# Kernel tuning notes

Measured on AMD Instinct MI355X. Metric: run time of the kernel, lower is better.

The kernel has to match this reference:

```python
import jax, jax.numpy as jnp
import numpy as np

N_NODES = 50000


def gcn_conv(x, W, b, edge_index, n):
    """PyG GCNConv with add_self_loops=True, normalize=True (symmetric norm)."""
    loop = jnp.arange(n, dtype=edge_index.dtype)
    row = jnp.concatenate([edge_index[0], loop])  # source
    col = jnp.concatenate([edge_index[1], loop])  # target
    ones = jnp.ones(row.shape[0], dtype=x.dtype)
    deg = jax.ops.segment_sum(ones, col, num_segments=n)
    dinv = jnp.where(deg > 0, jax.lax.rsqrt(deg), 0.0)
    norm = dinv[row] * dinv[col]  # [E+N]
    h = x @ W  # [N, hidden]
    out = jax.ops.segment_sum(h[row] * norm[:, None], col, num_segments=n)
    return out + b


def hgcn_forward(x, ei_ppi, ei_go, W0_ppi, b0_ppi, W0_go, b0_go,
                 W1_ppi, b1_ppi, W1_go, b1_go, Wc, bc, cand_edge_index):
    n = x.shape[0]
    # layer 0: HeteroConv(aggr='mean') over the two relations, then ReLU
    h = 0.5 * (gcn_conv(x, W0_ppi, b0_ppi, ei_ppi, n)
               + gcn_conv(x, W0_go, b0_go, ei_go, n))
    h = jax.nn.relu(h)
    # layer 1
    h = 0.5 * (gcn_conv(h, W1_ppi, b1_ppi, ei_ppi, n)
               + gcn_conv(h, W1_go, b1_go, ei_go, n))
    z = jax.nn.relu(h)  # [N, hidden]
    src, dst = cand_edge_index
    h_pair = jnp.concatenate([z[src], z[dst]], axis=1)  # [P, 2*hidden]
    logits = h_pair @ Wc + bc
    return z, jax.nn.sigmoid(logits)


def setup_inputs() -> dict:
    key = jax.random.key(0)
    ks = jax.random.split(key, 12)
    n, in_dim, hid, out_dim, E, P = N_NODES, 256, 128, 2, 1_000_000, 131072
    s = 1.0 / np.sqrt(in_dim)
    s2 = 1.0 / np.sqrt(hid)
    sc = 1.0 / np.sqrt(2 * hid)
    return {
        "x": jax.random.normal(ks[0], (n, in_dim), jnp.float32),
        "ei_ppi": jax.random.randint(ks[1], (2, E), 0, n, jnp.int32),
        "ei_go": jax.random.randint(ks[2], (2, E), 0, n, jnp.int32),
        "cand_edge_index": jax.random.randint(ks[3], (2, P), 0, n, jnp.int32),
        "W0_ppi": jax.random.normal(ks[4], (in_dim, hid), jnp.float32) * s,
        "b0_ppi": jnp.zeros((hid,), jnp.float32),
        "W0_go": jax.random.normal(ks[5], (in_dim, hid), jnp.float32) * s,
        "b0_go": jnp.zeros((hid,), jnp.float32),
        "W1_ppi": jax.random.normal(ks[6], (hid, hid), jnp.float32) * s2,
        "b1_ppi": jnp.zeros((hid,), jnp.float32),
        "W1_go": jax.random.normal(ks[7], (hid, hid), jnp.float32) * s2,
        "b1_go": jnp.zeros((hid,), jnp.float32),
        "Wc": jax.random.normal(ks[8], (2 * hid, out_dim), jnp.float32) * sc,
        "bc": jnp.zeros((out_dim,), jnp.float32),
    }


def reference(x, ei_ppi, ei_go, cand_edge_index, W0_ppi, b0_ppi, W0_go, b0_go,
              W1_ppi, b1_ppi, W1_go, b1_go, Wc, bc):
    return hgcn_forward(x, ei_ppi, ei_go, W0_ppi, b0_ppi, W0_go, b0_go,
                        W1_ppi, b1_ppi, W1_go, b1_go, Wc, bc, cand_edge_index)
```

## Files before the change

### kernel.cpp

```cpp
#include <hip/hip_runtime.h>
#include <math.h>

typedef _Float16 f16;
typedef f16  f16x2 __attribute__((ext_vector_type(2)));
typedef f16  f16x8 __attribute__((ext_vector_type(8)));
typedef float f32x4 __attribute__((ext_vector_type(4)));

#define CAP 64
#define CHK 96

__global__ __launch_bounds__(256) void prep3_kernel(
        int* __restrict__ cnt_p, const int* __restrict__ cols_p, const int* __restrict__ rows_p, int E1,
        int* __restrict__ cnt_g, const int* __restrict__ cols_g, const int* __restrict__ rows_g, int E2,
        unsigned short* __restrict__ buf_p, unsigned short* __restrict__ buf_g,
        const float* __restrict__ x, f16* __restrict__ xh, int x8,
        const float* __restrict__ W0p, const float* __restrict__ W0g,
        const float* __restrict__ W1p, const float* __restrict__ W1g,
        f16* __restrict__ T0p, f16* __restrict__ T0g,
        f16* __restrict__ T1p, f16* __restrict__ T1g,
        f16* __restrict__ zrow_p, f16* __restrict__ zrow_g,
        int XB, int n) {
    const int b = blockIdx.x;
    const int EBLK = 2 * CHK * 8;
    if (b < EBLK) {
        const int owner   = b & 7;
        const int pairIdx = b >> 3;
        const int sel     = (pairIdx >= CHK);
        const int chunk   = pairIdx - (sel ? CHK : 0);
        const int* cols = sel ? cols_g : cols_p;
        const int* rows = sel ? rows_g : rows_p;
        int* cnt = sel ? cnt_g : cnt_p;
        unsigned short* buf = sel ? buf_g : buf_p;
        const int E = sel ? E2 : E1;
        const int csz  = (((E + CHK - 1) / CHK) + 3) & ~3;
        const int s    = chunk * csz;
        const int eend = (s + csz < E) ? (s + csz) : E;
        if (s >= E) return;
        const int rlo = (int)((size_t)owner * n / 8);
        const int rhi = (int)((size_t)(owner + 1) * n / 8);
        const int vecEnd = s + ((eend - s) & ~3);
        for (int e = s + threadIdx.x * 4; e < vecEnd; e += 1024) {
            int4 c4 = *(const int4*)(cols + e);
            int4 r4 = *(const int4*)(rows + e);
            if (c4.x >= rlo && c4.x < rhi) {
                int p = atomicAdd(&cnt[c4.x], 1);
                if (p < CAP) buf[(size_t)c4.x * CAP + p] = (unsigned short)r4.x;
            }
            if (c4.y >= rlo && c4.y < rhi) {
                int p = atomicAdd(&cnt[c4.y], 1);
                if (p < CAP) buf[(size_t)c4.y * CAP + p] = (unsigned short)r4.y;
            }
            if (c4.z >= rlo && c4.z < rhi) {
                int p = atomicAdd(&cnt[c4.z], 1);
                if (p < CAP) buf[(size_t)c4.z * CAP + p] = (unsigned short)r4.z;
            }
            if (c4.w >= rlo && c4.w < rhi) {
                int p = atomicAdd(&cnt[c4.w], 1);
                if (p < CAP) buf[(size_t)c4.w * CAP + p] = (unsigned short)r4.w;
            }
        }
        for (int e = vecEnd + threadIdx.x; e < eend; e += 256) {
            int c = cols[e];
            if (c >= rlo && c < rhi) {
                int p = atomicAdd(&cnt[c], 1);
                if (p < CAP) buf[(size_t)c * CAP + p] = (unsigned short)rows[e];
            }
        }
    } else if (b < EBLK + XB) {
        int i = (b - EBLK) * 256 + threadIdx.x;
        if (i < x8) {
            const float4* p = (const float4*)(x + (size_t)i * 8);
            float4 a = p[0], c = p[1];
            f16x8 v = { (f16)a.x, (f16)a.y, (f16)a.z, (f16)a.w,
                        (f16)c.x, (f16)c.y, (f16)c.z, (f16)c.w };
            *(f16x8*)(xh + (size_t)i * 8) = v;
        }
    } else {
        int idx = (b - EBLK - XB) * 256 + threadIdx.x;
        if (idx < 98304) {
            const float* W; f16* T; int K; int local;
            if (idx < 32768)      { W = W0p; T = T0p; K = 256; local = idx; }
            else if (idx < 65536) { W = W0g; T = T0g; K = 256; local = idx - 32768; }
            else if (idx < 81920) { W = W1p; T = T1p; K = 128; local = idx - 65536; }
            else                  { W = W1g; T = T1g; K = 128; local = idx - 81920; }
            int k = local >> 7, nn = local & 127;
            T[(size_t)nn * K + k] = (f16)W[local];
        } else if (idx < 98304 + 256) {
            int t = idx - 98304;
            f16x8 zv = {};
            if (t < 16)       *(f16x8*)(zrow_p + t * 8) = zv;
            else if (t < 32)  *(f16x8*)(zrow_g + (t - 16) * 8) = zv;
        }
    }
}

__global__ __launch_bounds__(256) void gemm_dual_kernel(const f16* __restrict__ A,
        const f16* __restrict__ Btp, const f16* __restrict__ Btg,
        const int* __restrict__ cnt_p, const int* __restrict__ cnt_g,
        f16* __restrict__ Cp, f16* __restrict__ Cg, int M, int K) {
    const int wave = threadIdx.x >> 6;
    const int lane = threadIdx.x & 63;
    const int m    = lane & 15;
    const int kq   = lane >> 4;
    const int row0 = blockIdx.x * 64 + wave * 16;

    int arow = row0 + m; if (arow >= M) arow = M - 1;
    const f16* ap = A + (size_t)arow * K + kq * 8;

    f32x4 accp[8], accg[8];
    #pragma unroll
    for (int t = 0; t < 8; t++) {
        accp[t] = (f32x4){0.0f, 0.0f, 0.0f, 0.0f};
        accg[t] = (f32x4){0.0f, 0.0f, 0.0f, 0.0f};
    }
    for (int k0 = 0; k0 < K; k0 += 32) {
        f16x8 a = *(const f16x8*)(ap + k0);
        #pragma unroll
        for (int t = 0; t < 8; t++) {
            f16x8 bp = *(const f16x8*)(Btp + (size_t)(t * 16 + m) * K + k0 + kq * 8);
            accp[t] = __builtin_amdgcn_mfma_f32_16x16x32_f16(a, bp, accp[t], 0, 0, 0);
            f16x8 bg = *(const f16x8*)(Btg + (size_t)(t * 16 + m) * K + k0 + kq * 8);
            accg[t] = __builtin_amdgcn_mfma_f32_16x16x32_f16(a, bg, accg[t], 0, 0, 0);
        }
    }
    #pragma unroll
    for (int r = 0; r < 4; r++) {
        int row = row0 + kq * 4 + r;
        if (row < M) {
            float sp = rsqrtf(1.0f + (float)cnt_p[row]);
            float sg = rsqrtf(1.0f + (float)cnt_g[row]);
            #pragma unroll
            for (int t = 0; t < 8; t++) {
                Cp[(size_t)row * 128 + t * 16 + m] = (f16)(accp[t][r] * sp);
                Cg[(size_t)row * 128 + t * 16 + m] = (f16)(accg[t][r] * sg);
            }
        }
    }
}

template<int OUTF32>
__global__ __launch_bounds__(256) void fused_agg_kernel(
        const f16* __restrict__ Ap, const f16* __restrict__ Ag,
        const int* __restrict__ cnt_p, const unsigned short* __restrict__ buf_p,
        const int* __restrict__ cnt_g, const unsigned short* __restrict__ buf_g,
        const float* __restrict__ b_p, const float* __restrict__ b_g,
        float* __restrict__ outf, f16* __restrict__ outh, f16* __restrict__ outh2, int n) {
    const int wave = (blockIdx.x * blockDim.x + threadIdx.x) >> 6;
    const int lane = threadIdx.x & 63;
    if (wave >= n) return;
    const int c  = wave;
    const int g  = lane >> 4;
    const int sl = lane & 15;
    const size_t fo = (size_t)sl * 8;

    float ap[8] = {}, ag[8] = {};

    {
        const unsigned short* bp = buf_p + (size_t)c * CAP;
        int deg = cnt_p[c]; if (deg > CAP) deg = CAP;
        int i = 0;
        for (; i + 8 <= deg; i += 8) {
            int r0 = bp[i + g];
            int r1 = bp[i + 4 + g];
            f16x8 v0 = *(const f16x8*)(Ap + (size_t)r0 * 128 + fo);
            f16x8 v1 = *(const f16x8*)(Ap + (size_t)r1 * 128 + fo);
            #pragma unroll
            for (int k = 0; k < 8; k++) ap[k] += (float)v0[k] + (float)v1[k];
        }
        for (; i < deg; i += 4) {
            int j = i + g;
            int r = (j < deg) ? (int)bp[j] : n;
            f16x8 v = *(const f16x8*)(Ap + (size_t)r * 128 + fo);
            #pragma unroll
            for (int k = 0; k < 8; k++) ap[k] += (float)v[k];
        }
    }
    {
        const unsigned short* bg = buf_g + (size_t)c * CAP;
        int deg = cnt_g[c]; if (deg > CAP) deg = CAP;
        int i = 0;
        for (; i + 8 <= deg; i += 8) {
            int r0 = bg[i + g];
            int r1 = bg[i + 4 + g];
            f16x8 v0 = *(const f16x8*)(Ag + (size_t)r0 * 128 + fo);
            f16x8 v1 = *(const f16x8*)(Ag + (size_t)r1 * 128 + fo);
            #pragma unroll
            for (int k = 0; k < 8; k++) ag[k] += (float)v0[k] + (float)v1[k];
        }
        for (; i < deg; i += 4) {
            int j = i + g;
            int r = (j < deg) ? (int)bg[j] : n;
            f16x8 v = *(const f16x8*)(Ag + (size_t)r * 128 + fo);
            #pragma unroll
            for (int k = 0; k < 8; k++) ag[k] += (float)v[k];
        }
    }

    #pragma unroll
    for (int k = 0; k < 8; k++) {
        ap[k] += __shfl_xor(ap[k], 16);
        ap[k] += __shfl_xor(ap[k], 32);
        ag[k] += __shfl_xor(ag[k], 16);
        ag[k] += __shfl_xor(ag[k], 32);
    }

    f16x8 selfp = *(const f16x8*)(Ap + (size_t)c * 128 + fo);
    f16x8 selfg = *(const f16x8*)(Ag + (size_t)c * 128 + fo);
    const float dpc = 0.5f * rsqrtf(1.0f + (float)cnt_p[c]);
    const float dgc = 0.5f * rsqrtf(1.0f + (float)cnt_g[c]);
    const float4* bp4 = (const float4*)(b_p + fo);
    const float4* bg4 = (const float4*)(b_g + fo);
    float4 bpa = bp4[0], bpb = bp4[1], bga = bg4[0], bgb = bg4[1];
    float bb[8] = { bpa.x + bga.x, bpa.y + bga.y, bpa.z + bga.z, bpa.w + bga.w,
                    bpb.x + bgb.x, bpb.y + bgb.y, bpb.z + bgb.z, bpb.w + bgb.w };
    float out8[8];
    #pragma unroll
    for (int k = 0; k < 8; k++) {
        float s = fmaf(dpc, ap[k] + (float)selfp[k],
                  fmaf(dgc, ag[k] + (float)selfg[k], 0.5f * bb[k]));
        out8[k] = fmaxf(s, 0.0f);
    }

    if (g == 0) {
        if (OUTF32) {
            float4 o0 = { out8[0], out8[1], out8[2], out8[3] };
            float4 o1 = { out8[4], out8[5], out8[6], out8[7] };
            float4* op = (float4*)(outf + (size_t)c * 128 + fo);
            op[0] = o0; op[1] = o1;
            f16x8 oh = { (f16)out8[0], (f16)out8[1], (f16)out8[2], (f16)out8[3],
                         (f16)out8[4], (f16)out8[5], (f16)out8[6], (f16)out8[7] };
            *(f16x8*)(outh2 + (size_t)c * 128 + fo) = oh;
        } else {
            f16x8 oh = { (f16)out8[0], (f16)out8[1], (f16)out8[2], (f16)out8[3],
                         (f16)out8[4], (f16)out8[5], (f16)out8[6], (f16)out8[7] };
            *(f16x8*)(outh + (size_t)c * 128 + fo) = oh;
        }
    }
}

__global__ void pair_kernel(const f16* __restrict__ zh,
                            const int* __restrict__ src, const int* __restrict__ dst,
                            const float* __restrict__ Wc, const float* __restrict__ bc,
                            float* __restrict__ out, int P) {
    const int lane = threadIdx.x & 63;
    const int gwave = (blockIdx.x * blockDim.x + threadIdx.x) >> 6;
    if (gwave >= P) return;
    const int s = src[gwave];
    const int d = dst[gwave];
    f16x2 zs = *(const f16x2*)(zh + (size_t)s * 128 + lane * 2);
    f16x2 zd = *(const f16x2*)(zh + (size_t)d * 128 + lane * 2);
    const int k0 = lane * 2, k1 = lane * 2 + 1;
    float zsx = (float)zs.x, zsy = (float)zs.y;
    float zdx = (float)zd.x, zdy = (float)zd.y;
    float l0 = zsx * Wc[k0 * 2 + 0] + zsy * Wc[k1 * 2 + 0]
             + zdx * Wc[(128 + k0) * 2 + 0] + zdy * Wc[(128 + k1) * 2 + 0];
    float l1 = zsx * Wc[k0 * 2 + 1] + zsy * Wc[k1 * 2 + 1]
             + zdx * Wc[(128 + k0) * 2 + 1] + zdy * Wc[(128 + k1) * 2 + 1];
    #pragma unroll
    for (int off = 32; off >= 1; off >>= 1) {
        l0 += __shfl_down(l0, off);
        l1 += __shfl_down(l1, off);
    }
    if (lane == 0) {
        out[(size_t)gwave * 2 + 0] = 1.0f / (1.0f + expf(-(l0 + bc[0])));
        out[(size_t)gwave * 2 + 1] = 1.0f / (1.0f + expf(-(l1 + bc[1])));
    }
}

extern "C" void kernel_launch(void* const* d_in, const int* in_sizes, int n_in,
                              void* d_out, int out_size, void* d_ws, size_t ws_size,
                              hipStream_t stream) {
    const float* x      = (const float*)d_in[0];
    const int*   ei_ppi = (const int*)d_in[1];
    const int*   ei_go  = (const int*)d_in[2];
    const int*   cand   = (const int*)d_in[3];
    const float* W0_ppi = (const float*)d_in[4];
    const float* b0_ppi = (const float*)d_in[5];
    const float* W0_go  = (const float*)d_in[6];
    const float* b0_go  = (const float*)d_in[7];
    const float* W1_ppi = (const float*)d_in[8];
    const float* b1_ppi = (const float*)d_in[9];
    const float* W1_go  = (const float*)d_in[10];
    const float* b1_go  = (const float*)d_in[11];
    const float* Wc     = (const float*)d_in[12];
    const float* bc     = (const float*)d_in[13];

    const int n  = in_sizes[0] / 256;
    const int E1 = in_sizes[1] / 2;
    const int E2 = in_sizes[2] / 2;
    const int P  = in_sizes[3] / 2;

    float* z     = (float*)d_out;
    float* probs = z + (size_t)n * 128;

    const int* ppi_rows = ei_ppi;
    const int* ppi_cols = ei_ppi + E1;
    const int* go_rows  = ei_go;
    const int* go_cols  = ei_go + E2;

    const int x8 = n * 32;
    const int XB = (x8 + 255) / 256;
    const int WB = (98304 + 256 + 255) / 256;
    const int GB = (n + 63) / 64;
    const int aggGrid = (n + 3) / 4;
    const int EBLK = 2 * CHK * 8;

    size_t o = 0;
    float* ws = (float*)d_ws;
    int*   cnt_p  = (int*)(ws + o);   o += n;
    int*   cnt_g  = (int*)(ws + o);   o += n;
    unsigned short* buf_p = (unsigned short*)(ws + o);  o += (size_t)CAP * n / 2;
    unsigned short* buf_g = (unsigned short*)(ws + o);  o += (size_t)CAP * n / 2;
    f16*   Wt0p   = (f16*)(ws + o);   o += 256 * 128 / 2;
    f16*   Wt0g   = (f16*)(ws + o);   o += 256 * 128 / 2;
    f16*   Wt1p   = (f16*)(ws + o);   o += 128 * 128 / 2;
    f16*   Wt1g   = (f16*)(ws + o);   o += 128 * 128 / 2;
    f16*   xh     = (f16*)(ws + o);   o += (size_t)n * 256 / 2;
    f16*   A_p    = (f16*)(ws + o);   o += ((size_t)n + 1) * 128 / 2;
    f16*   A_g    = (f16*)(ws + o);   o += ((size_t)n + 1) * 128 / 2;
    f16*   h      = xh;
    f16*   zh     = xh + (size_t)n * 128;

    hipMemsetAsync(cnt_p, 0, (size_t)2 * n * sizeof(int), stream);
    prep3_kernel<<<EBLK + XB + WB, 256, 0, stream>>>(
        cnt_p, ppi_cols, ppi_rows, E1, cnt_g, go_cols, go_rows, E2,
        buf_p, buf_g, x, xh, x8,
        W0_ppi, W0_go, W1_ppi, W1_go, Wt0p, Wt0g, Wt1p, Wt1g,
        A_p + (size_t)n * 128, A_g + (size_t)n * 128, XB, n);
    gemm_dual_kernel<<<GB, 256, 0, stream>>>(xh, Wt0p, Wt0g, cnt_p, cnt_g, A_p, A_g, n, 256);
    fused_agg_kernel<0><<<aggGrid, 256, 0, stream>>>(A_p, A_g, cnt_p, buf_p,
                                                     cnt_g, buf_g,
                                                     b0_ppi, b0_go, nullptr, h, nullptr, n);
    gemm_dual_kernel<<<GB, 256, 0, stream>>>(h, Wt1p, Wt1g, cnt_p, cnt_g, A_p, A_g, n, 128);
    fused_agg_kernel<1><<<aggGrid, 256, 0, stream>>>(A_p, A_g, cnt_p, buf_p,
                                                     cnt_g, buf_g,
                                                     b1_ppi, b1_go, z, nullptr, zh, n);
    pair_kernel<<<(P + 3) / 4, 256, 0, stream>>>(zh, cand, cand + P, Wc, bc, probs, P);
}
```

Baseline: 392.1 us.

## Fuse x fp32-to-fp16 conversion into GEMM, use nontemporal edge loads, widen pair kernel

Removes the separate x→f16 conversion pass from the prep kernel. The first GEMM now reads fp32 x directly with nontemporal loads and converts to f16 in registers, which avoids writing and re-reading a 25 MB f16 copy. Edge-index reads in the bucketing pass use nontemporal loads. The pair kernel now handles two pairs per wave with 16-byte loads and a 32-lane xor reduction instead of 2-element loads per lane. The cost is twice the A-operand read bytes inside the GEMM, and the prep kernel may now finish faster since it no longer does the conversion.

Result: slower. 405.3 us (+3.4%).

```diff
diff --git a/kernel.cpp b/kernel.cpp
--- a/kernel.cpp
+++ b/kernel.cpp
@@ -5,21 +5,22 @@
 typedef f16  f16x2 __attribute__((ext_vector_type(2)));
 typedef f16  f16x8 __attribute__((ext_vector_type(8)));
 typedef float f32x4 __attribute__((ext_vector_type(4)));
+typedef int   int4v  __attribute__((ext_vector_type(4)));
+typedef float flt4v  __attribute__((ext_vector_type(4)));
 
 #define CAP 64
 #define CHK 96
 
-__global__ __launch_bounds__(256) void prep3_kernel(
+__global__ __launch_bounds__(256) void prep4_kernel(
         int* __restrict__ cnt_p, const int* __restrict__ cols_p, const int* __restrict__ rows_p, int E1,
         int* __restrict__ cnt_g, const int* __restrict__ cols_g, const int* __restrict__ rows_g, int E2,
         unsigned short* __restrict__ buf_p, unsigned short* __restrict__ buf_g,
-        const float* __restrict__ x, f16* __restrict__ xh, int x8,
         const float* __restrict__ W0p, const float* __restrict__ W0g,
         const float* __restrict__ W1p, const float* __restrict__ W1g,
         f16* __restrict__ T0p, f16* __restrict__ T0g,
         f16* __restrict__ T1p, f16* __restrict__ T1g,
         f16* __restrict__ zrow_p, f16* __restrict__ zrow_g,
-        int XB, int n) {
+        int n) {
     const int b = blockIdx.x;
     const int EBLK = 2 * CHK * 8;
     if (b < EBLK) {
@@ -40,8 +41,8 @@
         const int rhi = (int)((size_t)(owner + 1) * n / 8);
         const int vecEnd = s + ((eend - s) & ~3);
         for (int e = s + threadIdx.x * 4; e < vecEnd; e += 1024) {
-            int4 c4 = *(const int4*)(cols + e);
-            int4 r4 = *(const int4*)(rows + e);
+            int4v c4 = __builtin_nontemporal_load((const int4v*)(cols + e));
+            int4v r4 = __builtin_nontemporal_load((const int4v*)(rows + e));
             if (c4.x >= rlo && c4.x < rhi) {
                 int p = atomicAdd(&cnt[c4.x], 1);
                 if (p < CAP) buf[(size_t)c4.x * CAP + p] = (unsigned short)r4.x;
@@ -66,17 +67,8 @@
                 if (p < CAP) buf[(size_t)c * CAP + p] = (unsigned short)rows[e];
             }
         }
-    } else if (b < EBLK + XB) {
-        int i = (b - EBLK) * 256 + threadIdx.x;
-        if (i < x8) {
-            const float4* p = (const float4*)(x + (size_t)i * 8);
-            float4 a = p[0], c = p[1];
-            f16x8 v = { (f16)a.x, (f16)a.y, (f16)a.z, (f16)a.w,
-                        (f16)c.x, (f16)c.y, (f16)c.z, (f16)c.w };
-            *(f16x8*)(xh + (size_t)i * 8) = v;
-        }
     } else {
-        int idx = (b - EBLK - XB) * 256 + threadIdx.x;
+        int idx = (b - EBLK) * 256 + threadIdx.x;
         if (idx < 98304) {
             const float* W; f16* T; int K; int local;
             if (idx < 32768)      { W = W0p; T = T0p; K = 256; local = idx; }
@@ -94,7 +86,8 @@
     }
 }
 
-__global__ __launch_bounds__(256) void gemm_dual_kernel(const f16* __restrict__ A,
+template<int AF32>
+__global__ __launch_bounds__(256) void gemm_dual_kernel(const void* __restrict__ A_,
         const f16* __restrict__ Btp, const f16* __restrict__ Btg,
         const int* __restrict__ cnt_p, const int* __restrict__ cnt_g,
         f16* __restrict__ Cp, f16* __restrict__ Cg, int M, int K) {
@@ -105,7 +98,6 @@
     const int row0 = blockIdx.x * 64 + wave * 16;
 
     int arow = row0 + m; if (arow >= M) arow = M - 1;
-    const f16* ap = A + (size_t)arow * K + kq * 8;
 
     f32x4 accp[8], accg[8];
     #pragma unroll
@@ -113,8 +105,19 @@
         accp[t] = (f32x4){0.0f, 0.0f, 0.0f, 0.0f};
         accg[t] = (f32x4){0.0f, 0.0f, 0.0f, 0.0f};
     }
+    const float* af = (const float*)A_ + (size_t)arow * K + kq * 8;
+    const f16*   ah = (const f16*)A_   + (size_t)arow * K + kq * 8;
+
     for (int k0 = 0; k0 < K; k0 += 32) {
-        f16x8 a = *(const f16x8*)(ap + k0);
+        f16x8 a;
+        if (AF32) {
+            flt4v u = __builtin_nontemporal_load((const flt4v*)(af + k0));
+            flt4v v = __builtin_nontemporal_load((const flt4v*)(af + k0 + 4));
+            a = (f16x8){ (f16)u.x, (f16)u.y, (f16)u.z, (f16)u.w,
+                         (f16)v.x, (f16)v.y, (f16)v.z, (f16)v.w };
+        } else {
+            a = *(const f16x8*)(ah + k0);
+        }
         #pragma unroll
         for (int t = 0; t < 8; t++) {
             f16x8 bp = *(const f16x8*)(Btp + (size_t)(t * 16 + m) * K + k0 + kq * 8);
@@ -238,32 +241,34 @@
     }
 }
 
-__global__ void pair_kernel(const f16* __restrict__ zh,
+__global__ __launch_bounds__(256) void pair_kernel(const f16* __restrict__ zh,
                             const int* __restrict__ src, const int* __restrict__ dst,
                             const float* __restrict__ Wc, const float* __restrict__ bc,
                             float* __restrict__ out, int P) {
     const int lane = threadIdx.x & 63;
-    const int gwave = (blockIdx.x * blockDim.x + threadIdx.x) >> 6;
-    if (gwave >= P) return;
-    const int s = src[gwave];
-    const int d = dst[gwave];
-    f16x2 zs = *(const f16x2*)(zh + (size_t)s * 128 + lane * 2);
-    f16x2 zd = *(const f16x2*)(zh + (size_t)d * 128 + lane * 2);
-    const int k0 = lane * 2, k1 = lane * 2 + 1;
-    float zsx = (float)zs.x, zsy = (float)zs.y;
-    float zdx = (float)zd.x, zdy = (float)zd.y;
-    float l0 = zsx * Wc[k0 * 2 + 0] + zsy * Wc[k1 * 2 + 0]
-             + zdx * Wc[(128 + k0) * 2 + 0] + zdy * Wc[(128 + k1) * 2 + 0];
-    float l1 = zsx * Wc[k0 * 2 + 1] + zsy * Wc[k1 * 2 + 1]
-             + zdx * Wc[(128 + k0) * 2 + 1] + zdy * Wc[(128 + k1) * 2 + 1];
-    #pragma unroll
-    for (int off = 32; off >= 1; off >>= 1) {
-        l0 += __shfl_down(l0, off);
-        l1 += __shfl_down(l1, off);
-    }
-    if (lane == 0) {
-        out[(size_t)gwave * 2 + 0] = 1.0f / (1.0f + expf(-(l0 + bc[0])));
-        out[(size_t)gwave * 2 + 1] = 1.0f / (1.0f + expf(-(l1 + bc[1])));
+    const int wid  = (blockIdx.x * blockDim.x + threadIdx.x) >> 6;
+    const int q    = lane >> 4;
+    const int sl   = lane & 15;
+    const int pr   = wid * 2 + (q >> 1);
+    if (pr >= P) return;
+    const int node = (q & 1) ? dst[pr] : src[pr];
+    f16x8 zv = *(const f16x8*)(zh + (size_t)node * 128 + sl * 8);
+    const int kbase = (q & 1) * 128 + sl * 8;
+    float l0 = 0.0f, l1 = 0.0f;
+    #pragma unroll
+    for (int k = 0; k < 8; k++) {
+        float zk = (float)zv[k];
+        l0 = fmaf(zk, Wc[(kbase + k) * 2 + 0], l0);
+        l1 = fmaf(zk, Wc[(kbase + k) * 2 + 1], l1);
+    }
+    #pragma unroll
+    for (int off = 1; off <= 16; off <<= 1) {
+        l0 += __shfl_xor(l0, off);
+        l1 += __shfl_xor(l1, off);
+    }
+    if ((lane & 31) == 0) {
+        out[(size_t)pr * 2 + 0] = 1.0f / (1.0f + expf(-(l0 + bc[0])));
+        out[(size_t)pr * 2 + 1] = 1.0f / (1.0f + expf(-(l1 + bc[1])));
     }
 }
 
@@ -298,8 +303,6 @@
     const int* go_rows  = ei_go;
     const int* go_cols  = ei_go + E2;
 
-    const int x8 = n * 32;
-    const int XB = (x8 + 255) / 256;
     const int WB = (98304 + 256 + 255) / 256;
     const int GB = (n + 63) / 64;
     const int aggGrid = (n + 3) / 4;
@@ -315,25 +318,24 @@
     f16*   Wt0g   = (f16*)(ws + o);   o += 256 * 128 / 2;
     f16*   Wt1p   = (f16*)(ws + o);   o += 128 * 128 / 2;
     f16*   Wt1g   = (f16*)(ws + o);   o += 128 * 128 / 2;
-    f16*   xh     = (f16*)(ws + o);   o += (size_t)n * 256 / 2;
+    f16*   h      = (f16*)(ws + o);   o += (size_t)n * 128 / 2;
+    f16*   zh     = (f16*)(ws + o);   o += (size_t)n * 128 / 2;
     f16*   A_p    = (f16*)(ws + o);   o += ((size_t)n + 1) * 128 / 2;
     f16*   A_g    = (f16*)(ws + o);   o += ((size_t)n + 1) * 128 / 2;
-    f16*   h      = xh;
-    f16*   zh     = xh + (size_t)n * 128;
 
     hipMemsetAsync(cnt_p, 0, (size_t)2 * n * sizeof(int), stream);
-    prep3_kernel<<<EBLK + XB + WB, 256, 0, stream>>>(
+    prep4_kernel<<<EBLK + WB, 256, 0, stream>>>(
         cnt_p, ppi_cols, ppi_rows, E1, cnt_g, go_cols, go_rows, E2,
-        buf_p, buf_g, x, xh, x8,
+        buf_p, buf_g,
         W0_ppi, W0_go, W1_ppi, W1_go, Wt0p, Wt0g, Wt1p, Wt1g,
-        A_p + (size_t)n * 128, A_g + (size_t)n * 128, XB, n);
-    gemm_dual_kernel<<<GB, 256, 0, stream>>>(xh, Wt0p, Wt0g, cnt_p, cnt_g, A_p, A_g, n, 256);
+        A_p + (size_t)n * 128, A_g + (size_t)n * 128, n);
+    gemm_dual_kernel<1><<<GB, 256, 0, stream>>>(x, Wt0p, Wt0g, cnt_p, cnt_g, A_p, A_g, n, 256);
     fused_agg_kernel<0><<<aggGrid, 256, 0, stream>>>(A_p, A_g, cnt_p, buf_p,
                                                      cnt_g, buf_g,
                                                      b0_ppi, b0_go, nullptr, h, nullptr, n);
-    gemm_dual_kernel<<<GB, 256, 0, stream>>>(h, Wt1p, Wt1g, cnt_p, cnt_g, A_p, A_g, n, 128);
+    gemm_dual_kernel<0><<<GB, 256, 0, stream>>>(h, Wt1p, Wt1g, cnt_p, cnt_g, A_p, A_g, n, 128);
     fused_agg_kernel<1><<<aggGrid, 256, 0, stream>>>(A_p, A_g, cnt_p, buf_p,
                                                      cnt_g, buf_g,
                                                      b1_ppi, b1_go, z, nullptr, zh, n);
-    pair_kernel<<<(P + 3) / 4, 256, 0, stream>>>(zh, cand, cand + P, Wc, bc, probs, P);
-}
+    pair_kernel<<<(P + 1) / 2, 256, 0, stream>>>(zh, cand, cand + P, Wc, bc, probs, P);
+}
```
